# Performance work log

Measured on AMD Instinct MI355X. Metric: run time of the kernel, lower is better.

The kernel has to match this reference:

```python
import jax, jax.numpy as jnp
import numpy as np

B, N, D_IN, D_MODEL, N_HEAD = 4, 2048, 256, 256, 8
D_HEAD = D_MODEL // N_HEAD


def setup_inputs() -> dict:
    key = jax.random.key(0)
    ks = jax.random.split(key, 12)

    def lin(k, fan_in, fan_out):
        bound = 1.0 / np.sqrt(fan_in)
        kw, kb = jax.random.split(k)
        W = jax.random.uniform(kw, (fan_in, fan_out), jnp.float32, -bound, bound)
        b = jax.random.uniform(kb, (fan_out,), jnp.float32, -bound, bound)
        return W, b

    x = jax.random.normal(ks[0], (B, N, D_IN), jnp.float32)
    adj = jax.random.randint(ks[1], (B, N, N), 0, 2, jnp.int32)
    mask = jnp.ones((B, N), dtype=bool)

    Wq, bq = lin(ks[2], D_IN, D_MODEL)
    Wk, bk = lin(ks[3], D_IN, D_MODEL)
    Wv, bv = lin(ks[4], D_IN, D_MODEL)
    Wo, bo = lin(ks[5], D_MODEL, D_MODEL)
    Wl, bl = lin(ks[6], D_IN, D_MODEL)   # self.linear
    Wgi, bgi = lin(ks[7], D_IN, D_MODEL)  # GlobalNode.linear_gi
    Wgo, bgo = lin(ks[8], D_MODEL, D_MODEL)  # GlobalNode.linear_go

    return {"x": x, "adj": adj, "mask": mask,
            "Wq": Wq, "bq": bq, "Wk": Wk, "bk": bk, "Wv": Wv, "bv": bv,
            "Wo": Wo, "bo": bo, "Wl": Wl, "bl": bl,
            "Wgi": Wgi, "bgi": bgi, "Wgo": Wgo, "bgo": bgo}


def reference(x, adj, mask,
              Wq, bq, Wk, bk, Wv, bv, Wo, bo,
              Wl, bl, Wgi, bgi, Wgo, bgo):
    graph_mask = adj != 0  # [B, N, N]

    # multi-head attention, graph-masked
    q = (x @ Wq + bq).reshape(B, N, N_HEAD, D_HEAD)
    k = (x @ Wk + bk).reshape(B, N, N_HEAD, D_HEAD)
    v = (x @ Wv + bv).reshape(B, N, N_HEAD, D_HEAD)
    scores = jnp.einsum("bnhd,bmhd->bhnm", q, k) / jnp.sqrt(
        jnp.asarray(D_HEAD, x.dtype))
    scores = jnp.where(graph_mask[:, None, :, :], scores,
                       jnp.asarray(-1e9, x.dtype))
    attn = jax.nn.softmax(scores, axis=-1)  # [B, H, N, N]
    ctx = jnp.einsum("bhnm,bmhd->bnhd", attn, v).reshape(B, N, D_MODEL)
    h_gcn = ctx @ Wo + bo

    # linear fuse
    h = (x @ Wl + bl) + h_gcn

    # global node pooling
    mf = mask.astype(x.dtype)  # [B, N]
    docu_len = mf.sum(axis=1)  # [B]
    h_g = jnp.sum(jnp.tanh(x @ Wgi + bgi) * mf[:, :, None], axis=1)
    h_g = h_g / docu_len[:, None]
    h_g = h_g @ Wgo + bgo  # [B, D_MODEL]

    h = h + h_g[:, None, :]
    return jax.nn.elu(h)
```

## Files before the change

### kernel.cpp

```cpp
#include <hip/hip_runtime.h>

#define NB 4
#define NN 2048
#define ND 256
#define NH 8
#define DH 32
#define NTOK (NB * NN)

typedef short short4v __attribute__((ext_vector_type(4)));
typedef short short8 __attribute__((ext_vector_type(8)));
typedef float f32x4 __attribute__((ext_vector_type(4)));

#define QSC (0.17677669529663687f * 1.4426950408889634f)
#define FIXM 16.0f

__device__ __forceinline__ float b2f(short s) {
  union { unsigned u; float f; } c;
  c.u = ((unsigned)(unsigned short)s) << 16;
  return c.f;
}
__device__ __forceinline__ short f2b(float f) {
  union { float f; unsigned u; } c; c.f = f;
  unsigned u = c.u + 0x7fffu + ((c.u >> 16) & 1u);
  return (short)(u >> 16);
}
__device__ __forceinline__ short f2bt(float f) {
  union { float f; unsigned u; } c; c.f = f;
  return (short)(c.u >> 16);
}
__device__ __forceinline__ float ex2(float x) {
#if __has_builtin(__builtin_amdgcn_exp2f)
  return __builtin_amdgcn_exp2f(x);
#else
  return exp2f(x);
#endif
}

struct TPtrs {
  const float* src[6];
  short* dst[6];
};

__global__ __launch_bounds__(256) void prep(const int* __restrict__ adj,
                                            unsigned long long* __restrict__ adjbT,
                                            const float* __restrict__ x,
                                            short* __restrict__ xb, TPtrs tp) {
  __shared__ float tile[16][17];
  const int bid = blockIdx.x;
  const int t = threadIdx.x;
  if (bid < NTOK) {
    const int wv = t >> 6, l = t & 63;
    const int b_ = bid >> 11, n = bid & (NN - 1);
    const int* ap = adj + (size_t)bid * NN;
#pragma unroll
    for (int c = wv; c < NN / 64; c += 4) {
      unsigned long long m = __ballot(ap[c * 64 + l] != 0);
      if (l == 0) adjbT[((size_t)(b_ * (NN / 64) + c)) * NN + n] = m;
    }
  } else if (bid < NTOK + NTOK * ND / (256 * 8)) {
    const int i = ((bid - NTOK) * 256 + t) * 8;
    const float4 a = *(const float4*)&x[i];
    const float4 b = *(const float4*)&x[i + 4];
    short8 o;
    o[0] = f2b(a.x); o[1] = f2b(a.y); o[2] = f2b(a.z); o[3] = f2b(a.w);
    o[4] = f2b(b.x); o[5] = f2b(b.y); o[6] = f2b(b.z); o[7] = f2b(b.w);
    *(short8*)&xb[i] = o;
  } else {
    const int tt = bid - NTOK - NTOK * ND / (256 * 8);
    const int wi = tt >> 8, rem = tt & 255;
    const int r0 = (rem >> 4) * 16, c0 = (rem & 15) * 16;
    const int ty = t >> 4, tx = t & 15;
    tile[ty][tx] = tp.src[wi][(r0 + ty) * ND + c0 + tx];
    __syncthreads();
    tp.dst[wi][(c0 + ty) * ND + r0 + tx] = f2b(tile[tx][ty]);
  }
}

struct PPtrs {
  const short* WT[5];
  const float* bias[5];
  void* out[5];
};

__global__ __launch_bounds__(256) void proj5(const short* __restrict__ X, PPtrs p) {
  __shared__ short As[64][264];
  const int bm = blockIdx.x, bn = blockIdx.y, z = blockIdx.z;
  const int t = threadIdx.x;
  const short* Xb = X + (size_t)bm * 64 * ND;
#pragma unroll
  for (int c = t; c < 64 * 32; c += 256) {
    int r = c >> 5, co = (c & 31) << 3;
    *(short8*)&As[r][co] = *(const short8*)&Xb[r * ND + co];
  }
  __syncthreads();
  const int w = t >> 6, l = t & 63;
  const int wr = (w >> 1) * 32, wc = (w & 1) * 32;
  const int lr = l & 15, lg = l >> 4;
  const short* WT = p.WT[z];
  f32x4 acc[2][2] = {};
#pragma unroll
  for (int ks = 0; ks < 8; ++ks) {
    short8 a[2], bb[2];
#pragma unroll
    for (int m = 0; m < 2; ++m)
      a[m] = *(const short8*)&As[wr + m * 16 + lr][ks * 32 + lg * 8];
#pragma unroll
    for (int n = 0; n < 2; ++n)
      bb[n] = *(const short8*)&WT[(size_t)(bn * 64 + wc + n * 16 + lr) * ND +
                                  ks * 32 + lg * 8];
#pragma unroll
    for (int m = 0; m < 2; ++m)
#pragma unroll
      for (int n = 0; n < 2; ++n)
        acc[m][n] =
            __builtin_amdgcn_mfma_f32_16x16x32_bf16(a[m], bb[n], acc[m][n], 0, 0, 0);
  }
  const float* bias = p.bias[z];
  void* outp = p.out[z];
#pragma unroll
  for (int m = 0; m < 2; ++m)
#pragma unroll
    for (int n = 0; n < 2; ++n) {
      const int col = bn * 64 + wc + n * 16 + lr;
      const float bv = bias[col];
      const int row0 = bm * 64 + wr + m * 16 + lg * 4;
      if (z == 2) {
        short4v o;
#pragma unroll
        for (int j = 0; j < 4; ++j) o[j] = f2b(acc[m][n][j] + bv);
        const int bb_ = row0 >> 11, n0 = row0 & (NN - 1);
        const int hh = col >> 5, dd = col & (DH - 1);
        *(short4v*)&((short*)outp)[((size_t)((bb_ * NH + hh) * DH + dd)) * NN + n0] = o;
      } else {
#pragma unroll
        for (int j = 0; j < 4; ++j) {
          const int row = row0 + j;
          const size_t idx = (size_t)row * ND + col;
          float v = acc[m][n][j] + bv;
          if (z == 4) v = tanhf(v);
          if (z == 0) v *= QSC;
          if (z == 3)
            ((float*)outp)[idx] = v;
          else
            ((short*)outp)[idx] = f2b(v);
        }
      }
    }
}

__global__ __launch_bounds__(256) void proj_final(
    const short* __restrict__ X, const short* __restrict__ WT,
    const float* __restrict__ bias, float* outp,
    const float* linf, const float* __restrict__ hg) {
  __shared__ short As[64][264];
  const int bm = blockIdx.x, bn = blockIdx.y;
  const int t = threadIdx.x;
  const short* Xb = X + (size_t)bm * 64 * ND;
#pragma unroll
  for (int c = t; c < 64 * 32; c += 256) {
    int r = c >> 5, co = (c & 31) << 3;
    *(short8*)&As[r][co] = *(const short8*)&Xb[r * ND + co];
  }
  __syncthreads();
  const int w = t >> 6, l = t & 63;
  const int wr = (w >> 1) * 32, wc = (w & 1) * 32;
  const int lr = l & 15, lg = l >> 4;
  f32x4 acc[2][2] = {};
#pragma unroll
  for (int ks = 0; ks < 8; ++ks) {
    short8 a[2], bb[2];
#pragma unroll
    for (int m = 0; m < 2; ++m)
      a[m] = *(const short8*)&As[wr + m * 16 + lr][ks * 32 + lg * 8];
#pragma unroll
    for (int n = 0; n < 2; ++n)
      bb[n] = *(const short8*)&WT[(size_t)(bn * 64 + wc + n * 16 + lr) * ND +
                                  ks * 32 + lg * 8];
#pragma unroll
    for (int m = 0; m < 2; ++m)
#pragma unroll
      for (int n = 0; n < 2; ++n)
        acc[m][n] =
            __builtin_amdgcn_mfma_f32_16x16x32_bf16(a[m], bb[n], acc[m][n], 0, 0, 0);
  }
#pragma unroll
  for (int m = 0; m < 2; ++m)
#pragma unroll
    for (int n = 0; n < 2; ++n) {
      const int col = bn * 64 + wc + n * 16 + lr;
      const float bv = bias[col];
#pragma unroll
      for (int j = 0; j < 4; ++j) {
        const int row = bm * 64 + wr + m * 16 + lg * 4 + j;
        const size_t idx = (size_t)row * ND + col;
        float v = acc[m][n][j] + bv + linf[idx] + hg[(row >> 11) * ND + col];
        v = v > 0.f ? v : expm1f(v);
        outp[idx] = v;
      }
    }
}

__global__ __launch_bounds__(256) void pool_partial(const short* __restrict__ gi,
                                                    float* __restrict__ part) {
  const int b = blockIdx.y, ch = blockIdx.x, d = threadIdx.x;
  const short* p = gi + ((size_t)b * NN + ch * 128) * ND + d;
  float a = 0.f;
  for (int r = 0; r < 128; ++r) a += b2f(p[r * ND]);
  part[(b * 16 + ch) * ND + d] = a;
}

__global__ __launch_bounds__(256) void hg_kernel(const float* __restrict__ part,
                                                 const float* __restrict__ Wgo,
                                                 const float* __restrict__ bgo,
                                                 float* __restrict__ hg) {
  __shared__ float gs[ND];
  const int b = blockIdx.x, d2 = threadIdx.x;
  float a = 0.f;
#pragma unroll
  for (int i = 0; i < 16; ++i) a += part[(b * 16 + i) * ND + d2];
  gs[d2] = a * (1.0f / (float)NN);
  __syncthreads();
  float acc = bgo[d2];
  for (int d = 0; d < ND; ++d) acc += gs[d] * Wgo[d * ND + d2];
  hg[b * ND + d2] = acc;
}

struct APtrs {
  short* op[4];
  float* ml;
};

__global__ __launch_bounds__(256) void attn9(
    const short* __restrict__ q, const short* __restrict__ k,
    const short* __restrict__ vt, const unsigned long long* __restrict__ adjbT,
    APtrs ap_, int iters, int KS) {
  const int chunk = blockIdx.x, qb = blockIdx.y;
  const int ksi = chunk % KS, b = chunk / KS;
  const int wid = threadIdx.x >> 6, l = threadIdx.x & 63;
  const int h = blockIdx.z * 4 + wid;
  const int lr = l & 15, lg = l >> 4;
  const size_t bN = (size_t)b * NN;
  const int q0 = qb * 128;

  short8 qf[8];
#pragma unroll
  for (int qh = 0; qh < 8; ++qh)
    qf[qh] = *(const short8*)&q[(bN + q0 + qh * 16 + lr) * ND + h * DH + lg * 8];

  const short* kb = k + bN * ND + h * DH;
  const short* vtb = vt + (size_t)(b * NH + h) * DH * NN;
  const unsigned long long* abT = adjbT + (size_t)(b * (NN / 64)) * NN + q0;
  short* opart = ap_.op[ksi];
  float* mlp = ap_.ml + (size_t)ksi * NTOK * NH * 2;

  f32x4 oacc[8][2] = {};
  float lrun[8];
#pragma unroll
  for (int i = 0; i < 8; ++i) lrun[i] = 0.f;

  const int it0 = ksi * iters;
  for (int it = it0; it < it0 + iters; ++it) {
    const int k0 = it * 64;
    unsigned long long w8[8];
#pragma unroll
    for (int qh = 0; qh < 8; ++qh)
      w8[qh] = abT[(size_t)it * NN + qh * 16 + lr];
    short8 kf[2][2];
#pragma unroll
    for (int t32 = 0; t32 < 2; ++t32)
#pragma unroll
      for (int m = 0; m < 2; ++m)
        kf[t32][m] =
            *(const short8*)&kb[(size_t)(k0 + t32 * 32 + m * 16 + lr) * ND + lg * 8];
    short8 vf[2][2];
#pragma unroll
    for (int t32 = 0; t32 < 2; ++t32)
#pragma unroll
      for (int dh = 0; dh < 2; ++dh) {
        const short* vr = &vtb[(size_t)(dh * 16 + lr) * NN + k0 + t32 * 32 + lg * 4];
        const short4v vlo = *(const short4v*)vr;
        const short4v vhi = *(const short4v*)(vr + 16);
        short8 tv;
#pragma unroll
        for (int j = 0; j < 4; ++j) { tv[j] = vlo[j]; tv[4 + j] = vhi[j]; }
        vf[t32][dh] = tv;
      }
#pragma unroll
    for (int qq = 0; qq < 4; ++qq) {
      f32x4 S[2][2][2];
      __builtin_amdgcn_s_setprio(1);
#pragma unroll
      for (int qh2 = 0; qh2 < 2; ++qh2)
#pragma unroll
        for (int t32 = 0; t32 < 2; ++t32)
#pragma unroll
          for (int m = 0; m < 2; ++m)
            S[qh2][t32][m] = __builtin_amdgcn_mfma_f32_16x16x32_bf16(
                kf[t32][m], qf[qq * 2 + qh2], (f32x4){0.f, 0.f, 0.f, 0.f}, 0, 0, 0);
      __builtin_amdgcn_s_setprio(0);
#pragma unroll
      for (int qh2 = 0; qh2 < 2; ++qh2) {
        const int qh = qq * 2 + qh2;
        const unsigned long long w = w8[qh] >> (lg * 4);
        float ts = 0.f;
        short8 pf[2];
#pragma unroll
        for (int t32 = 0; t32 < 2; ++t32) {
          short8 pp;
#pragma unroll
          for (int m = 0; m < 2; ++m)
#pragma unroll
            for (int jj = 0; jj < 4; ++jj) {
              const float e = ex2(S[qh2][t32][m][jj] - FIXM);
              const bool on = (w >> (t32 * 32 + m * 16 + jj)) & 1ull;
              const float p = on ? e : 0.f;
              ts += p;
              pp[m * 4 + jj] = f2bt(p);
            }
          pf[t32] = pp;
        }
        ts += __shfl_xor(ts, 16, 64);
        ts += __shfl_xor(ts, 32, 64);
        lrun[qh] += ts;
        __builtin_amdgcn_s_setprio(1);
#pragma unroll
        for (int t32 = 0; t32 < 2; ++t32)
#pragma unroll
          for (int dh = 0; dh < 2; ++dh)
            oacc[qh][dh] = __builtin_amdgcn_mfma_f32_16x16x32_bf16(
                vf[t32][dh], pf[t32], oacc[qh][dh], 0, 0, 0);
        __builtin_amdgcn_s_setprio(0);
      }
    }
  }
#pragma unroll
  for (int qh = 0; qh < 8; ++qh) {
    const int row = q0 + qh * 16 + lr;
    if (lg == 0) {
      float2 v; v.x = FIXM; v.y = lrun[qh];
      *(float2*)&mlp[((size_t)(b * NN + row) * NH + h) * 2] = v;
    }
    const size_t rowb = (size_t)(bN + row) * ND + h * DH;
#pragma unroll
    for (int dh = 0; dh < 2; ++dh) {
      short4v o;
#pragma unroll
      for (int jj = 0; jj < 4; ++jj) o[jj] = f2b(oacc[qh][dh][jj]);
      *(short4v*)&opart[rowb + dh * 16 + lg * 4] = o;
    }
  }
}

struct CPtrs {
  const short* op[4];
  const float* ml;
};

__global__ __launch_bounds__(256) void combine_k(CPtrs cp, short* __restrict__ ctx,
                                                 int ks) {
  const int idx = blockIdx.x * 256 + threadIdx.x;
  const int token = idx >> 5;
  const int sub = idx & 31;
  const int h = sub >> 2, d8 = (sub & 3) * 8;
  float m[4], li[4];
  float M = -INFINITY;
  for (int c = 0; c < ks; ++c) {
    const float2 v = *(const float2*)&cp.ml[(((size_t)c * NTOK + token) * NH + h) * 2];
    m[c] = v.x; li[c] = v.y;
    M = fmaxf(M, v.x);
  }
  float L = 0.f, fc[4];
  for (int c = 0; c < ks; ++c) {
    fc[c] = ex2(m[c] - M);
    L += li[c] * fc[c];
  }
  const float inv = 1.0f / L;
  float o[8];
#pragma unroll
  for (int j = 0; j < 8; ++j) o[j] = 0.f;
  for (int c = 0; c < ks; ++c) {
    const short8 vv = *(const short8*)&cp.op[c][(size_t)token * ND + h * DH + d8];
#pragma unroll
    for (int j = 0; j < 8; ++j) o[j] += b2f(vv[j]) * fc[c];
  }
  short8 ov;
#pragma unroll
  for (int j = 0; j < 8; ++j) ov[j] = f2b(o[j] * inv);
  *(short8*)&ctx[(size_t)token * ND + h * DH + d8] = ov;
}

extern "C" void kernel_launch(void* const* d_in, const int* in_sizes, int n_in,
                              void* d_out, int out_size, void* d_ws,
                              size_t ws_size, hipStream_t stream) {
  const float* x = (const float*)d_in[0];
  const int* adj = (const int*)d_in[1];
  const int wb = (in_sizes[2] == NB * NN) ? 3 : 2;
  const float* Wq = (const float*)d_in[wb + 0];
  const float* bq = (const float*)d_in[wb + 1];
  const float* Wk = (const float*)d_in[wb + 2];
  const float* bk = (const float*)d_in[wb + 3];
  const float* Wv = (const float*)d_in[wb + 4];
  const float* bv = (const float*)d_in[wb + 5];
  const float* Wo = (const float*)d_in[wb + 6];
  const float* bo = (const float*)d_in[wb + 7];
  const float* Wl = (const float*)d_in[wb + 8];
  const float* bl = (const float*)d_in[wb + 9];
  const float* Wgi = (const float*)d_in[wb + 10];
  const float* bgi = (const float*)d_in[wb + 11];
  const float* Wgo = (const float*)d_in[wb + 12];
  const float* bgo = (const float*)d_in[wb + 13];

  short* WT = (short*)d_ws;
  short* WqT = WT + 0 * 65536;
  short* WkT = WT + 1 * 65536;
  short* WvT = WT + 2 * 65536;
  short* WoT = WT + 3 * 65536;
  short* WlT = WT + 4 * 65536;
  short* WgiT = WT + 5 * 65536;
  short* xb = WT + 6 * 65536;
  short* qb_ = xb + (size_t)NTOK * ND;
  short* kb_ = qb_ + (size_t)NTOK * ND;
  short* vtb = kb_ + (size_t)NTOK * ND;
  short* gib = vtb + (size_t)NTOK * ND;
  unsigned long long* adjbT = (unsigned long long*)(gib + (size_t)NTOK * ND);
  float* part = (float*)(adjbT + (size_t)NTOK * (NN / 64));
  float* hgb = part + NB * 16 * ND;
  float* mlbase = hgb + NB * ND;
  const size_t fixed_bytes = (size_t)((char*)mlbase - (char*)d_ws);
  int KS = 1;
  for (int cand = 4; cand >= 1; cand >>= 1) {
    const size_t need = fixed_bytes + (size_t)cand * NTOK * NH * 2 * 4 +
                        (size_t)(cand - 1) * NTOK * ND * 2;
    if (need <= ws_size) { KS = cand; break; }
  }
  short* opex = (short*)(mlbase + (size_t)KS * NTOK * NH * 2);
  short* ctxb = xb;
  float* linf = (float*)d_out;

  APtrs ap;
  ap.op[0] = gib;
  for (int c = 1; c < 4; ++c)
    ap.op[c] = (c < KS) ? (opex + (size_t)(c - 1) * NTOK * ND) : gib;
  ap.ml = mlbase;

  TPtrs tp;
  tp.src[0] = Wq; tp.src[1] = Wk; tp.src[2] = Wv;
  tp.src[3] = Wo; tp.src[4] = Wl; tp.src[5] = Wgi;
  tp.dst[0] = WqT; tp.dst[1] = WkT; tp.dst[2] = WvT;
  tp.dst[3] = WoT; tp.dst[4] = WlT; tp.dst[5] = WgiT;
  prep<<<NTOK + NTOK * ND / (256 * 8) + 6 * 256, 256, 0, stream>>>(adj, adjbT, x,
                                                                   xb, tp);

  PPtrs pp;
  pp.WT[0] = WqT; pp.WT[1] = WkT; pp.WT[2] = WvT; pp.WT[3] = WlT; pp.WT[4] = WgiT;
  pp.bias[0] = bq; pp.bias[1] = bk; pp.bias[2] = bv; pp.bias[3] = bl; pp.bias[4] = bgi;
  pp.out[0] = qb_; pp.out[1] = kb_; pp.out[2] = vtb; pp.out[3] = linf; pp.out[4] = gib;
  proj5<<<dim3(NTOK / 64, ND / 64, 5), 256, 0, stream>>>(xb, pp);

  pool_partial<<<dim3(16, NB), 256, 0, stream>>>(gib, part);
  hg_kernel<<<NB, 256, 0, stream>>>(part, Wgo, bgo, hgb);

  attn9<<<dim3(NB * KS, NN / 128, 2), 256, 0, stream>>>(qb_, kb_, vtb, adjbT, ap,
                                                        (NN / 64) / KS, KS);

  CPtrs cp;
  for (int c = 0; c < 4; ++c) cp.op[c] = ap.op[c];
  cp.ml = mlbase;
  combine_k<<<NTOK * NH * 4 / 256, 256, 0, stream>>>(cp, ctxb, KS);

  proj_final<<<dim3(NTOK / 64, ND / 64), 256, 0, stream>>>(ctxb, WoT, bo,
                                                           (float*)d_out, linf, hgb);
}
```

Measured before the change: 145.6 us.

## Regroup attention blocks by head, compute row sums via MFMA with ones

```diff
diff --git a/kernel.cpp b/kernel.cpp
--- a/kernel.cpp
+++ b/kernel.cpp
@@ -12,7 +12,6 @@
 typedef float f32x4 __attribute__((ext_vector_type(4)));
 
 #define QSC (0.17677669529663687f * 1.4426950408889634f)
-#define FIXM 16.0f
 
 __device__ __forceinline__ float b2f(short s) {
   union { unsigned u; float f; } c;
@@ -230,22 +229,26 @@
   float* ml;
 };
 
-__global__ __launch_bounds__(256) void attn9(
+__global__ __launch_bounds__(512) void attn10(
     const short* __restrict__ q, const short* __restrict__ k,
     const short* __restrict__ vt, const unsigned long long* __restrict__ adjbT,
     APtrs ap_, int iters, int KS) {
-  const int chunk = blockIdx.x, qb = blockIdx.y;
+  const int chunk = blockIdx.x;
   const int ksi = chunk % KS, b = chunk / KS;
+  const int h = blockIdx.y >> 1, qhalf = blockIdx.y & 1;
   const int wid = threadIdx.x >> 6, l = threadIdx.x & 63;
-  const int h = blockIdx.z * 4 + wid;
   const int lr = l & 15, lg = l >> 4;
   const size_t bN = (size_t)b * NN;
-  const int q0 = qb * 128;
+  const int q0 = qhalf * 1024 + wid * 128;
 
   short8 qf[8];
 #pragma unroll
   for (int qh = 0; qh < 8; ++qh)
     qf[qh] = *(const short8*)&q[(bN + q0 + qh * 16 + lr) * ND + h * DH + lg * 8];
+
+  short8 ones;
+#pragma unroll
+  for (int j = 0; j < 8; ++j) ones[j] = (short)0x3F80;
 
   const short* kb = k + bN * ND + h * DH;
   const short* vtb = vt + (size_t)(b * NH + h) * DH * NN;
@@ -254,12 +257,11 @@
   float* mlp = ap_.ml + (size_t)ksi * NTOK * NH * 2;
 
   f32x4 oacc[8][2] = {};
-  float lrun[8];
-#pragma unroll
-  for (int i = 0; i < 8; ++i) lrun[i] = 0.f;
+  f32x4 olacc[8] = {};
 
   const int it0 = ksi * iters;
   for (int it = it0; it < it0 + iters; ++it) {
+    __syncthreads();
     const int k0 = it * 64;
     unsigned long long w8[8];
 #pragma unroll
@@ -302,7 +304,6 @@
       for (int qh2 = 0; qh2 < 2; ++qh2) {
         const int qh = qq * 2 + qh2;
         const unsigned long long w = w8[qh] >> (lg * 4);
-        float ts = 0.f;
         short8 pf[2];
 #pragma unroll
         for (int t32 = 0; t32 < 2; ++t32) {
@@ -311,24 +312,22 @@
           for (int m = 0; m < 2; ++m)
 #pragma unroll
             for (int jj = 0; jj < 4; ++jj) {
-              const float e = ex2(S[qh2][t32][m][jj] - FIXM);
+              const float e = ex2(S[qh2][t32][m][jj]);
               const bool on = (w >> (t32 * 32 + m * 16 + jj)) & 1ull;
-              const float p = on ? e : 0.f;
-              ts += p;
-              pp[m * 4 + jj] = f2bt(p);
+              pp[m * 4 + jj] = on ? f2bt(e) : (short)0;
             }
           pf[t32] = pp;
         }
-        ts += __shfl_xor(ts, 16, 64);
-        ts += __shfl_xor(ts, 32, 64);
-        lrun[qh] += ts;
         __builtin_amdgcn_s_setprio(1);
 #pragma unroll
-        for (int t32 = 0; t32 < 2; ++t32)
+        for (int t32 = 0; t32 < 2; ++t32) {
 #pragma unroll
           for (int dh = 0; dh < 2; ++dh)
             oacc[qh][dh] = __builtin_amdgcn_mfma_f32_16x16x32_bf16(
                 vf[t32][dh], pf[t32], oacc[qh][dh], 0, 0, 0);
+          olacc[qh] = __builtin_amdgcn_mfma_f32_16x16x32_bf16(
+              ones, pf[t32], olacc[qh], 0, 0, 0);
+        }
         __builtin_amdgcn_s_setprio(0);
       }
     }
@@ -337,7 +336,7 @@
   for (int qh = 0; qh < 8; ++qh) {
     const int row = q0 + qh * 16 + lr;
     if (lg == 0) {
-      float2 v; v.x = FIXM; v.y = lrun[qh];
+      float2 v; v.x = 0.f; v.y = olacc[qh][0];
       *(float2*)&mlp[((size_t)(b * NN + row) * NH + h) * 2] = v;
     }
     const size_t rowb = (size_t)(bN + row) * ND + h * DH;
@@ -460,8 +459,8 @@
   pool_partial<<<dim3(16, NB), 256, 0, stream>>>(gib, part);
   hg_kernel<<<NB, 256, 0, stream>>>(part, Wgo, bgo, hgb);
 
-  attn9<<<dim3(NB * KS, NN / 128, 2), 256, 0, stream>>>(qb_, kb_, vtb, adjbT, ap,
-                                                        (NN / 64) / KS, KS);
+  attn10<<<dim3(NB * KS, NH * 2), 512, 0, stream>>>(qb_, kb_, vtb, adjbT, ap,
+                                                    (NN / 64) / KS, KS);
 
   CPtrs cp;
   for (int c = 0; c < 4; ++c) cp.op[c] = ap.op[c];
```

Measured after the change: 138.2 us. -5.1%, faster.
